# Kernel tuning notes

Measured on AMD Instinct MI355X. Metric: run time of the kernel, lower is better.

Reference implementation:

```python
import jax, jax.numpy as jnp
import numpy as np

SR = 16000
NFFT = 512
HOP = 160
D_MIC = 0.05
SPEED = 343.0
PRE = 0.97
ALPHA, BETA, GAMMA = 0.5, 0.3, 0.2
MAXLEN = 40000
N_ANGLES = 181
T = 6400000

# ---- constant buffers (match torch register_buffer setup) ----
_freqs = np.fft.rfftfreq(NFFT, 1.0 / SR).astype(np.float32)            # [F]
_angles = np.linspace(0.0, 180.0, N_ANGLES).astype(np.float32)         # [A]
_tau = -(D_MIC * np.cos(np.deg2rad(_angles))) / SPEED
_phase = (2.0 * np.pi) * _tau[:, None] * _freqs[None, :]               # [A, F]
STEER_R = jnp.asarray(np.cos(_phase).astype(np.float32))
STEER_I = jnp.asarray(np.sin(_phase).astype(np.float32))
ANGLE_GRID = jnp.asarray(_angles)

_wl = SPEED / (_freqs + 1e-6)
_sr_res = D_MIC / _wl
_spatial = 1.0 / (1.0 + np.exp(-4.0 * (_sr_res - 0.1)))
_fw = 1.0 - np.exp(-((_freqs - SR / 6.0) ** 2) / (2.0 * (SR / 4.0) ** 2))
_alias = np.where(_sr_res < 0.5, np.ones_like(_freqs), np.exp(-2.0 * (_sr_res - 0.5) ** 2))
_cw = (_spatial * _fw * _alias)[None, :]
FREQ_W = jnp.asarray((_cw / (_cw.sum() + 1e-6)).astype(np.float32))    # [1, F]

_w = np.exp(np.linspace(-2.0, 0.0, MAXLEN).astype(np.float32))
TEMPORAL = jnp.asarray((_w / _w.sum()).reshape(1, 1, -1))              # [1,1,MAXLEN]

_n = np.arange(NFFT)
WINDOW = jnp.asarray((0.5 - 0.5 * np.cos(2.0 * np.pi * _n / NFFT)).astype(np.float32))
N_FRAMES = (T - NFFT) // HOP + 1
FRAME_IDX = jnp.asarray((np.arange(N_FRAMES)[:, None] * HOP + _n[None, :]).astype(np.int32))


def _stft(x):
    # x: [1, 1, T] -> (real, imag) each [1, F, n_frames]
    frames = x[:, 0, :][:, FRAME_IDX] * WINDOW       # [1, n_frames, NFFT]
    spec = jnp.fft.rfft(frames, axis=-1)             # [1, n_frames, F]
    spec = jnp.swapaxes(spec, 1, 2)                  # [1, F, n_frames]
    return jnp.real(spec).astype(jnp.float32), jnp.imag(spec).astype(jnp.float32)


def _preproc(w):
    w = w * (1.0 / 32768.0)
    w = w - jnp.mean(w, axis=-1, keepdims=True)
    return jnp.concatenate([w[:, :, :1], w[:, :, 1:] - PRE * w[:, :, :-1]], axis=-1)


def _mvdr_scores(mic_wav_0, mic_wav_1):
    r0, i0 = _stft(_preproc(mic_wav_0))
    r1, i1 = _stft(_preproc(mic_wav_1))
    p0 = r0 * r0 + i0 * i0
    p1 = r1 * r1 + i1 * i1
    r01 = r0 * r1 + i0 * i1
    i01 = i0 * r1 - r0 * i1
    wts = TEMPORAL[..., : p0.shape[-1]]
    R00 = (p0 * wts).sum(2)                          # [1, F]
    R11 = (p1 * wts).sum(2)
    R01r = (r01 * wts).sum(2)
    R01i = (i01 * wts).sum(2)
    trace = (R00 + R11) * 0.5
    det = R00 * R11 - (R01r ** 2 + R01i ** 2) + 1e-6 * trace
    inv_det = 1.0 / det
    iR00 = R11 * inv_det
    iR11 = R00 * inv_det
    iR01r = -R01r * inv_det
    iR01i = -R01i * inv_det
    qf = iR01r * STEER_R + iR01i * STEER_I           # [A, F] (B=1 broadcast)
    qf = iR00 + iR11 + qf + qf
    mvdr = 1.0 / (qf + 1e-6)
    logp = jnp.log(mvdr + 1e-6)
    geometric = jnp.exp((logp * FREQ_W).sum(-1))     # [A]
    arithmetic = (mvdr * FREQ_W).sum(-1)
    peak_w = jax.nn.softmax(mvdr + mvdr, axis=-1)
    peak = (mvdr * peak_w * FREQ_W).sum(-1)
    return ALPHA * geometric + BETA * arithmetic + GAMMA * peak


def setup_inputs() -> dict:
    key = jax.random.key(0)
    k0, k1 = jax.random.split(key)
    mic_wav_0 = jax.random.normal(k0, (1, 1, T), jnp.float32) * 8000.0
    noise = jax.random.normal(k1, (1, 1, T), jnp.float32) * 8000.0
    # correlated second channel with a small time shift (plausible TDOA)
    mic_wav_1 = 0.7 * jnp.roll(mic_wav_0, 3, axis=-1) + 0.3 * noise
    return {"mic_wav_0": mic_wav_0, "mic_wav_1": mic_wav_1}


def reference(mic_wav_0, mic_wav_1):
    scores = _mvdr_scores(mic_wav_0, mic_wav_1)      # [A]
    return ANGLE_GRID[jnp.argmax(scores, axis=-1)]
```

## Files before the change

kernel.cpp:

```cpp
#include <hip/hip_runtime.h>
#include <math.h>

#ifndef M_PI
#define M_PI 3.14159265358979323846
#endif

#define HOP 160
#define NBM 1024
#define NBLK_MAX 1024

__device__ __forceinline__ float wave_reduce(float v) {
    for (int off = 32; off > 0; off >>= 1) v += __shfl_down(v, off, 64);
    return v;
}

__device__ __forceinline__ void dft8(float* xr, float* xi) {
    const float s = 0.70710678118654752440f;
    float t0r = xr[0] + xr[4], t0i = xi[0] + xi[4];
    float t1r = xr[0] - xr[4], t1i = xi[0] - xi[4];
    float t2r = xr[2] + xr[6], t2i = xi[2] + xi[6];
    float t3r = xr[2] - xr[6], t3i = xi[2] - xi[6];
    float E0r = t0r + t2r, E0i = t0i + t2i;
    float E2r = t0r - t2r, E2i = t0i - t2i;
    float E1r = t1r + t3i, E1i = t1i - t3r;
    float E3r = t1r - t3i, E3i = t1i + t3r;
    float u0r = xr[1] + xr[5], u0i = xi[1] + xi[5];
    float u1r = xr[1] - xr[5], u1i = xi[1] - xi[5];
    float u2r = xr[3] + xr[7], u2i = xi[3] + xi[7];
    float u3r = xr[3] - xr[7], u3i = xi[3] - xi[7];
    float O0r = u0r + u2r, O0i = u0i + u2i;
    float O2r = u0r - u2r, O2i = u0i - u2i;
    float O1r = u1r + u3i, O1i = u1i - u3r;
    float O3r = u1r - u3i, O3i = u1i + u3r;
    float T1r = s * (O1r + O1i), T1i = s * (O1i - O1r);
    float T2r = O2i,             T2i = -O2r;
    float T3r = s * (O3i - O3r), T3i = -s * (O3r + O3i);
    xr[0] = E0r + O0r; xi[0] = E0i + O0i;
    xr[4] = E0r - O0r; xi[4] = E0i - O0i;
    xr[1] = E1r + T1r; xi[1] = E1i + T1i;
    xr[5] = E1r - T1r; xi[5] = E1i - T1i;
    xr[2] = E2r + T2r; xi[2] = E2i + T2i;
    xr[6] = E2r - T2r; xi[6] = E2i - T2i;
    xr[3] = E3r + T3r; xi[3] = E3i + T3i;
    xr[7] = E3r - T3r; xi[7] = E3i - T3i;
}

__device__ __forceinline__ void cmul_t(float& zr, float& zi, float tr, float ti) {
    float r = zr * tr - zi * ti;
    float i = zr * ti + zi * tr;
    zr = r; zi = i;
}

__device__ __forceinline__ int stripe(int i) {
    return ((i >> 7) << 8) | (i & 127);
}

__global__ __launch_bounds__(256) void mean_partial_kernel(
        const float* __restrict__ x0, const float* __restrict__ x1,
        float* __restrict__ part, int n, int nbm)
{
    int tid = threadIdx.x;
    float s0 = 0.f, s1 = 0.f;
    int n4 = n >> 2;
    const float4* x04 = (const float4*)x0;
    const float4* x14 = (const float4*)x1;
    for (int i = blockIdx.x * blockDim.x + tid; i < n4; i += blockDim.x * gridDim.x) {
        float4 a = x04[i], b = x14[i];
        s0 += (a.x + a.y) + (a.z + a.w);
        s1 += (b.x + b.y) + (b.z + b.w);
    }
    __shared__ float red[4][2];
    s0 = wave_reduce(s0); s1 = wave_reduce(s1);
    int lane = tid & 63, w = tid >> 6;
    if (lane == 0) { red[w][0] = s0; red[w][1] = s1; }
    __syncthreads();
    if (tid == 0) {
        part[blockIdx.x]       = red[0][0] + red[1][0] + red[2][0] + red[3][0];
        part[nbm + blockIdx.x] = red[0][1] + red[1][1] + red[2][1] + red[3][1];
    }
}

__global__ __launch_bounds__(256) void mean_final_kernel(
        const float* __restrict__ part, float* __restrict__ means,
        float* __restrict__ twd, int n, int nbm)
{
    int tid = threadIdx.x;
    float v0 = 0.f, v1 = 0.f;
    for (int i = tid; i < nbm; i += 256) { v0 += part[i]; v1 += part[nbm + i]; }
    __shared__ float red[4][2];
    v0 = wave_reduce(v0); v1 = wave_reduce(v1);
    int lane = tid & 63, w = tid >> 6;
    if (lane == 0) { red[w][0] = v0; red[w][1] = v1; }
    __syncthreads();
    if (tid == 0) {
        float s0 = red[0][0] + red[1][0] + red[2][0] + red[3][0];
        float s1 = red[0][1] + red[1][1] + red[2][1] + red[3][1];
        float inv = 1.0f / ((float)n * 32768.0f);
        means[0] = s0 * inv;
        means[1] = s1 * inv;
    }
    if (tid < 64) {
        int l = tid, hi = l >> 3;
        for (int j = 0; j < 8; ++j) {
            twd[j * 64 + l] = 0.5f - 0.5f * cosf((float)(2.0 * M_PI / 512.0) * (float)(l + 64 * j));
            float c1, s1v, c2, s2v;
            sincosf((float)(-2.0 * M_PI / 64.0) * (float)(j * hi), &s1v, &c1);
            sincosf((float)(-2.0 * M_PI / 512.0) * (float)(j * l), &s2v, &c2);
            twd[(8 + j) * 64 + l]  = c1;
            twd[(16 + j) * 64 + l] = s1v;
            twd[(24 + j) * 64 + l] = c2;
            twd[(32 + j) * 64 + l] = s2v;
        }
    }
}

__global__ __launch_bounds__(256, 4) void stft_fft_kernel(
        const float* __restrict__ x0, const float* __restrict__ x1,
        const float* __restrict__ means, const float* __restrict__ twd,
        float* __restrict__ partials,
        int nframes, int fpb, int nblocks, float invS, float kslope)
{
    __shared__ float smem[4160];
    const int tid = threadIdx.x;
    const int w = tid >> 6, l = tid & 63;
    float* buf = smem + w * 1024;
    const int n0 = l & 7, hi = l >> 3;
    const int pl = (64 - l) & 63;

    float winv[8], t1r[8], t1i[8], t2r[8], t2i[8];
#pragma unroll
    for (int j = 0; j < 8; ++j) {
        winv[j] = twd[j * 64 + l];
        t1r[j]  = twd[(8 + j) * 64 + l];
        t1i[j]  = twd[(16 + j) * 64 + l];
        t2r[j]  = twd[(24 + j) * 64 + l];
        t2i[j]  = twd[(32 + j) * 64 + l];
    }
    const float m0 = means[0], m1 = means[1];
    const float cm0 = 0.03f * m0, cm1 = 0.03f * m1;
    const float k15 = 1.0f / 32768.0f;

    float A[8];
    float Wr[5], Wi[5];
#pragma unroll
    for (int r = 0; r < 8; ++r) A[r] = 0.f;
#pragma unroll
    for (int r = 0; r < 5; ++r) { Wr[r] = 0.f; Wi[r] = 0.f; }

    int f0 = blockIdx.x * fpb;
    int f1 = f0 + fpb; if (f1 > nframes) f1 = nframes;

    for (int f = f0 + w; f < f1; f += 4) {
        int base = f * HOP;
        float wt = expf(fmaf(kslope, (float)f, -2.0f)) * invS;

        float zr[8], zi[8];
#pragma unroll
        for (int j = 0; j < 8; ++j) {
            int t = base + l + 64 * j;
            int tp = t - 1;
            if (j == 0) tp = (tp < 0) ? 0 : tp;
            float d0 = fmaf(-0.97f, x0[tp], x0[t]);
            float d1 = fmaf(-0.97f, x1[tp], x1[t]);
            float y0 = fmaf(d0, k15, -cm0);
            float y1 = fmaf(d1, k15, -cm1);
            zr[j] = y0 * winv[j];
            zi[j] = y1 * winv[j];
        }

        dft8(zr, zi);

#pragma unroll
        for (int k2 = 0; k2 < 8; ++k2) {
            int a = stripe((l ^ (k2 << 3)) + 64 * k2);
            buf[a] = zr[k2]; buf[a + 128] = zi[k2];
        }
#pragma unroll
        for (int j = 0; j < 8; ++j) {
            int a = stripe(n0 + 8 * (j ^ hi) + 64 * hi);
            zr[j] = buf[a]; zi[j] = buf[a + 128];
        }
#pragma unroll
        for (int j = 1; j < 8; ++j) cmul_t(zr[j], zi[j], t1r[j], t1i[j]);
        dft8(zr, zi);

#pragma unroll
        for (int k1 = 0; k1 < 8; ++k1) {
            int a = stripe(hi + 8 * ((k1 ^ n0) + 8 * n0));
            buf[a] = zr[k1]; buf[a + 128] = zi[k1];
        }
#pragma unroll
        for (int j = 0; j < 8; ++j) {
            int a = stripe(n0 + 8 * ((hi ^ j) + 8 * j));
            zr[j] = buf[a]; zi[j] = buf[a + 128];
        }
#pragma unroll
        for (int j = 1; j < 8; ++j) cmul_t(zr[j], zi[j], t2r[j], t2i[j]);
        dft8(zr, zi);

#pragma unroll
        for (int r = 0; r < 8; ++r) {
            float u = fmaf(zr[r], zr[r], zi[r] * zi[r]);
            A[r] = fmaf(wt, u, A[r]);
        }
#pragma unroll
        for (int r = 0; r < 4; ++r) {
            float br = __shfl(zr[7 - r], pl, 64);
            float bi = __shfl(zi[7 - r], pl, 64);
            if (l == 0) { br = zr[(8 - r) & 7]; bi = zi[(8 - r) & 7]; }
            float wr = fmaf(zr[r], br, -(zi[r] * bi));
            float wi = fmaf(zr[r], bi, zi[r] * br);
            Wr[r] = fmaf(wt, wr, Wr[r]);
            Wi[r] = fmaf(wt, wi, Wi[r]);
        }
        {
            float wr = fmaf(zr[4], zr[4], -(zi[4] * zi[4]));
            float wi = 2.f * zr[4] * zi[4];
            Wr[4] = fmaf(wt, wr, Wr[4]);
            Wi[4] = fmaf(wt, wi, Wi[4]);
        }
    }

    float R00[4], R11[4], R01r[4], R01i[4];
#pragma unroll
    for (int r = 0; r < 4; ++r) {
        float ap = __shfl(A[7 - r], pl, 64);
        if (l == 0) ap = A[(8 - r) & 7];
        R00[r]  = 0.25f * (A[r] + ap + 2.f * Wr[r]);
        R11[r]  = 0.25f * (A[r] + ap - 2.f * Wr[r]);
        R01r[r] = 0.5f  * Wi[r];
        R01i[r] = 0.25f * (A[r] - ap);
    }

    __syncthreads();
    float (*red)[1028] = (float (*)[1028])smem;
#pragma unroll
    for (int r = 0; r < 4; ++r) {
        int k = l + 64 * r;
        red[w][0 * 257 + k] = R00[r];
        red[w][1 * 257 + k] = R11[r];
        red[w][2 * 257 + k] = R01r[r];
        red[w][3 * 257 + k] = R01i[r];
    }
    if (l == 0) {
        red[w][0 * 257 + 256] = 0.5f * (A[4] + Wr[4]);
        red[w][1 * 257 + 256] = 0.5f * (A[4] - Wr[4]);
        red[w][2 * 257 + 256] = 0.5f * Wi[4];
        red[w][3 * 257 + 256] = 0.f;
    }
    __syncthreads();
    for (int s = tid; s < 1028; s += 256) {
        float v = (red[0][s] + red[1][s]) + (red[2][s] + red[3][s]);
        partials[(size_t)s * nblocks + blockIdx.x] = v;
    }
}

__global__ __launch_bounds__(256) void reduce_kernel(
        const float* __restrict__ partials, float* __restrict__ R, int nblocks)
{
    int s = blockIdx.x;
    int tid = threadIdx.x, lane = tid & 63, w = tid >> 6;
    const float* p = partials + (size_t)s * nblocks;
    float v = 0.f;
    for (int i = tid; i < nblocks; i += 256) v += p[i];
    __shared__ float red[4];
    v = wave_reduce(v);
    if (lane == 0) red[w] = v;
    __syncthreads();
    if (tid == 0) R[s] = (red[0] + red[1]) + (red[2] + red[3]);
}

__global__ __launch_bounds__(64) void score_kernel(
        const float* __restrict__ R, float* __restrict__ scores)
{
    int a = blockIdx.x;
    int l = threadIdx.x;

    float rad = (float)a * (float)(M_PI / 180.0);
    float tau = -(0.05f * cosf(rad)) / 343.0f;
    float t2  = (float)(2.0 * M_PI) * tau;

    float fwsum = 0.f;
    float geo = 0.f, ari = 0.f;
    float m = -1e30f, se = 0.f, pe = 0.f;

    for (int q = 0; q < 5; ++q) {
        int kk = l + 64 * q;
        if (kk > 256) break;
        float R00  = R[0 * 257 + kk];
        float R11  = R[1 * 257 + kk];
        float R01r = R[2 * 257 + kk];
        float R01i = R[3 * 257 + kk];
        float trace = (R00 + R11) * 0.5f;
        float det = R00 * R11 - (R01r * R01r + R01i * R01i) + 1e-6f * trace;
        float inv_det = 1.0f / det;
        float Sd = (R11 + R00) * inv_det;
        float qr = -R01r * inv_det;
        float qi = -R01i * inv_det;

        float fq = 31.25f * (float)kk;
        float wl = 343.0f / (fq + 1e-6f);
        float sr = 0.05f / wl;
        float spatial = 1.0f / (1.0f + expf(-4.0f * (sr - 0.1f)));
        float d = fq - (float)(16000.0 / 6.0);
        float fwq = 1.0f - expf(-(d * d) / (float)(2.0 * 4000.0 * 4000.0));
        float alias = (sr < 0.5f) ? 1.0f : expf(-2.0f * (sr - 0.5f) * (sr - 0.5f));
        float fw = spatial * fwq * alias;
        fwsum += fw;

        float cr, ci;
        sincosf(t2 * fq, &ci, &cr);
        float t  = qr * cr + qi * ci;
        float qf = Sd + t + t;
        float mv = 1.0f / (qf + 1e-6f);

        geo = fmaf(logf(mv + 1e-6f), fw, geo);
        ari = fmaf(mv, fw, ari);
        float x = mv + mv;
        if (x > m) {
            float sc = expf(m - x);
            se = fmaf(se, sc, 1.0f);
            pe = fmaf(pe, sc, mv * fw);
            m = x;
        } else {
            float e = expf(x - m);
            se += e;
            pe = fmaf(mv * fw, e, pe);
        }
    }

    for (int off = 1; off < 64; off <<= 1) {
        fwsum += __shfl_xor(fwsum, off, 64);
        geo   += __shfl_xor(geo, off, 64);
        ari   += __shfl_xor(ari, off, 64);
        float mo = __shfl_xor(m, off, 64);
        float so = __shfl_xor(se, off, 64);
        float po = __shfl_xor(pe, off, 64);
        float mm = fmaxf(m, mo);
        float c1 = expf(m - mm), c2 = expf(mo - mm);
        se = fmaf(se, c1, so * c2);
        pe = fmaf(pe, c1, po * c2);
        m = mm;
    }
    if (l == 0) {
        float invcw = 1.0f / (fwsum + 1e-6f);
        float geon = geo * invcw;
        float arin = ari * invcw;
        float peak = (pe * invcw) / se;
        scores[a] = 0.5f * expf(geon) + 0.3f * arin + 0.2f * peak;
    }
}

__global__ __launch_bounds__(256) void argmax_kernel(
        const float* __restrict__ scores, float* __restrict__ out)
{
    int tid = threadIdx.x, lane = tid & 63, w = tid >> 6;
    float v = (tid < 181) ? scores[tid] : -1e30f;
    int   i = tid;
    for (int off = 1; off < 64; off <<= 1) {
        float vo = __shfl_xor(v, off, 64);
        int   io = __shfl_xor(i, off, 64);
        if (vo > v || (vo == v && io < i)) { v = vo; i = io; }
    }
    __shared__ float rv[4];
    __shared__ int   ri[4];
    if (lane == 0) { rv[w] = v; ri[w] = i; }
    __syncthreads();
    if (tid == 0) {
        float bv = rv[0]; int bi = ri[0];
        for (int q = 1; q < 4; ++q) {
            if (rv[q] > bv || (rv[q] == bv && ri[q] < bi)) { bv = rv[q]; bi = ri[q]; }
        }
        out[0] = (float)bi;
    }
}

extern "C" void kernel_launch(void* const* d_in, const int* in_sizes, int n_in,
                              void* d_out, int out_size, void* d_ws, size_t ws_size,
                              hipStream_t stream) {
    const float* x0 = (const float*)d_in[0];
    const float* x1 = (const float*)d_in[1];
    float* out = (float*)d_out;
    int T = in_sizes[0];
    int nframes = (T - 512) / HOP + 1;

    double S = 0.0;
    for (int j = 0; j < 40000; ++j) S += exp(-2.0 + 2.0 * (double)j / 39999.0);
    float invS = (float)(1.0 / S);
    float kslope = (float)(2.0 / 39999.0);

    float* ws = (float*)d_ws;
    float* means    = ws;
    float* twd      = ws + 64;
    float* mpart    = ws + 4096;
    float* Rbuf     = ws + 8192;
    float* scores   = ws + 9472;
    float* partials = ws + 16384;

    long availf = (long)(ws_size / 4) - 16384;
    int nblocks = (int)(availf / 1028);
    if (nblocks > NBLK_MAX) nblocks = NBLK_MAX;
    if (nblocks < 1) nblocks = 1;
    int fpb = (nframes + nblocks - 1) / nblocks;

    mean_partial_kernel<<<NBM, 256, 0, stream>>>(x0, x1, mpart, T, NBM);
    mean_final_kernel<<<1, 256, 0, stream>>>(mpart, means, twd, T, NBM);
    stft_fft_kernel<<<nblocks, 256, 0, stream>>>(x0, x1, means, twd, partials,
                                                 nframes, fpb, nblocks, invS, kslope);
    reduce_kernel<<<1028, 256, 0, stream>>>(partials, Rbuf, nblocks);
    score_kernel<<<181, 64, 0, stream>>>(Rbuf, scores);
    argmax_kernel<<<1, 256, 0, stream>>>(scores, out);
}
```

Before: 84.79 us.

## Fuse mean pass into STFT kernel and apply DC correction analytically in scoring

Removes the separate mean-reduction and twiddle-setup kernels. Each STFT block now sums its own chunk of the raw signal, and the STFT runs on the un-centred signal. The mean's effect on the covariance (only the DC bins and the window's neighbouring bins) is corrected afterwards in score_kernel, using accumulated weighted linear spectra and the total weight. Twiddles are now built by in-register recurrence from one sincos instead of table loads, and blocks and occupancy go up (NBLK_MAX 2048, launch bounds 256,8). This cuts one full pass over the input and two launches, at the cost of extra correction algebra and possible float accuracy drift from the twiddle recurrence and the uncentred FFT.

```diff
diff --git a/kernel.cpp b/kernel.cpp
--- a/kernel.cpp
+++ b/kernel.cpp
@@ -6,8 +6,8 @@
 #endif
 
 #define HOP 160
-#define NBM 1024
-#define NBLK_MAX 1024
+#define NBLK_MAX 2048
+#define PSLOTS 1036
 
 __device__ __forceinline__ float wave_reduce(float v) {
     for (int off = 32; off > 0; off >>= 1) v += __shfl_down(v, off, 64);
@@ -55,93 +55,44 @@
     return ((i >> 7) << 8) | (i & 127);
 }
 
-__global__ __launch_bounds__(256) void mean_partial_kernel(
+__global__ __launch_bounds__(256, 8) void stft_fft_kernel(
         const float* __restrict__ x0, const float* __restrict__ x1,
-        float* __restrict__ part, int n, int nbm)
+        float* __restrict__ partials,
+        int T, int nframes, int fpb, int nblocks, int cs,
+        float invS, float kslope)
 {
-    int tid = threadIdx.x;
-    float s0 = 0.f, s1 = 0.f;
-    int n4 = n >> 2;
-    const float4* x04 = (const float4*)x0;
-    const float4* x14 = (const float4*)x1;
-    for (int i = blockIdx.x * blockDim.x + tid; i < n4; i += blockDim.x * gridDim.x) {
-        float4 a = x04[i], b = x14[i];
-        s0 += (a.x + a.y) + (a.z + a.w);
-        s1 += (b.x + b.y) + (b.z + b.w);
-    }
-    __shared__ float red[4][2];
-    s0 = wave_reduce(s0); s1 = wave_reduce(s1);
-    int lane = tid & 63, w = tid >> 6;
-    if (lane == 0) { red[w][0] = s0; red[w][1] = s1; }
-    __syncthreads();
-    if (tid == 0) {
-        part[blockIdx.x]       = red[0][0] + red[1][0] + red[2][0] + red[3][0];
-        part[nbm + blockIdx.x] = red[0][1] + red[1][1] + red[2][1] + red[3][1];
-    }
-}
-
-__global__ __launch_bounds__(256) void mean_final_kernel(
-        const float* __restrict__ part, float* __restrict__ means,
-        float* __restrict__ twd, int n, int nbm)
-{
-    int tid = threadIdx.x;
-    float v0 = 0.f, v1 = 0.f;
-    for (int i = tid; i < nbm; i += 256) { v0 += part[i]; v1 += part[nbm + i]; }
-    __shared__ float red[4][2];
-    v0 = wave_reduce(v0); v1 = wave_reduce(v1);
-    int lane = tid & 63, w = tid >> 6;
-    if (lane == 0) { red[w][0] = v0; red[w][1] = v1; }
-    __syncthreads();
-    if (tid == 0) {
-        float s0 = red[0][0] + red[1][0] + red[2][0] + red[3][0];
-        float s1 = red[0][1] + red[1][1] + red[2][1] + red[3][1];
-        float inv = 1.0f / ((float)n * 32768.0f);
-        means[0] = s0 * inv;
-        means[1] = s1 * inv;
-    }
-    if (tid < 64) {
-        int l = tid, hi = l >> 3;
-        for (int j = 0; j < 8; ++j) {
-            twd[j * 64 + l] = 0.5f - 0.5f * cosf((float)(2.0 * M_PI / 512.0) * (float)(l + 64 * j));
-            float c1, s1v, c2, s2v;
-            sincosf((float)(-2.0 * M_PI / 64.0) * (float)(j * hi), &s1v, &c1);
-            sincosf((float)(-2.0 * M_PI / 512.0) * (float)(j * l), &s2v, &c2);
-            twd[(8 + j) * 64 + l]  = c1;
-            twd[(16 + j) * 64 + l] = s1v;
-            twd[(24 + j) * 64 + l] = c2;
-            twd[(32 + j) * 64 + l] = s2v;
-        }
-    }
-}
-
-__global__ __launch_bounds__(256, 4) void stft_fft_kernel(
-        const float* __restrict__ x0, const float* __restrict__ x1,
-        const float* __restrict__ means, const float* __restrict__ twd,
-        float* __restrict__ partials,
-        int nframes, int fpb, int nblocks, float invS, float kslope)
-{
-    __shared__ float smem[4160];
+    __shared__ float smem[4 * PSLOTS];
     const int tid = threadIdx.x;
     const int w = tid >> 6, l = tid & 63;
     float* buf = smem + w * 1024;
     const int n0 = l & 7, hi = l >> 3;
     const int pl = (64 - l) & 63;
 
-    float winv[8], t1r[8], t1i[8], t2r[8], t2i[8];
-#pragma unroll
-    for (int j = 0; j < 8; ++j) {
-        winv[j] = twd[j * 64 + l];
-        t1r[j]  = twd[(8 + j) * 64 + l];
-        t1i[j]  = twd[(16 + j) * 64 + l];
-        t2r[j]  = twd[(24 + j) * 64 + l];
-        t2i[j]  = twd[(32 + j) * 64 + l];
-    }
-    const float m0 = means[0], m1 = means[1];
-    const float cm0 = 0.03f * m0, cm1 = 0.03f * m1;
-    const float k15 = 1.0f / 32768.0f;
+    float c0 = 0.f, c1 = 0.f;
+    {
+        int lo = blockIdx.x * cs;
+        int hi2 = lo + cs; if (hi2 > T) hi2 = T;
+        for (int i = lo + tid; i < hi2; i += 256) { c0 += x0[i]; c1 += x1[i]; }
+        c0 = wave_reduce(c0); c1 = wave_reduce(c1);
+        if (l == 0) { smem[2 * w] = c0; smem[2 * w + 1] = c1; }
+    }
+    __syncthreads();
+    const float c0T = (smem[0] + smem[2]) + (smem[4] + smem[6]);
+    const float c1T = (smem[1] + smem[3]) + (smem[5] + smem[7]);
+    __syncthreads();
+
+    float winv[8];
+#pragma unroll
+    for (int j = 0; j < 8; ++j)
+        winv[j] = (0.5f - 0.5f * cosf((float)(2.0 * M_PI / 512.0) * (float)(l + 64 * j)))
+                  * (1.0f / 32768.0f);
+    float g1r, g1i, g2r, g2i;
+    sincosf((float)(-2.0 * M_PI / 64.0) * (float)hi, &g1i, &g1r);
+    sincosf((float)(-2.0 * M_PI / 512.0) * (float)l, &g2i, &g2r);
 
     float A[8];
     float Wr[5], Wi[5];
+    float L0r = 0.f, L0i = 0.f, L7r = 0.f, L7i = 0.f;
 #pragma unroll
     for (int r = 0; r < 8; ++r) A[r] = 0.f;
 #pragma unroll
@@ -162,10 +113,8 @@
             if (j == 0) tp = (tp < 0) ? 0 : tp;
             float d0 = fmaf(-0.97f, x0[tp], x0[t]);
             float d1 = fmaf(-0.97f, x1[tp], x1[t]);
-            float y0 = fmaf(d0, k15, -cm0);
-            float y1 = fmaf(d1, k15, -cm1);
-            zr[j] = y0 * winv[j];
-            zi[j] = y1 * winv[j];
+            zr[j] = d0 * winv[j];
+            zi[j] = d1 * winv[j];
         }
 
         dft8(zr, zi);
@@ -180,8 +129,18 @@
             int a = stripe(n0 + 8 * (j ^ hi) + 64 * hi);
             zr[j] = buf[a]; zi[j] = buf[a + 128];
         }
-#pragma unroll
-        for (int j = 1; j < 8; ++j) cmul_t(zr[j], zi[j], t1r[j], t1i[j]);
+        {
+            float rc = g1r, rs = g1i;
+#pragma unroll
+            for (int j = 1; j < 8; ++j) {
+                cmul_t(zr[j], zi[j], rc, rs);
+                if (j < 7) {
+                    float nr = rc * g1r - rs * g1i;
+                    rs = fmaf(rc, g1i, rs * g1r);
+                    rc = nr;
+                }
+            }
+        }
         dft8(zr, zi);
 
 #pragma unroll
@@ -194,8 +153,18 @@
             int a = stripe(n0 + 8 * ((hi ^ j) + 8 * j));
             zr[j] = buf[a]; zi[j] = buf[a + 128];
         }
-#pragma unroll
-        for (int j = 1; j < 8; ++j) cmul_t(zr[j], zi[j], t2r[j], t2i[j]);
+        {
+            float rc = g2r, rs = g2i;
+#pragma unroll
+            for (int j = 1; j < 8; ++j) {
+                cmul_t(zr[j], zi[j], rc, rs);
+                if (j < 7) {
+                    float nr = rc * g2r - rs * g2i;
+                    rs = fmaf(rc, g2i, rs * g2r);
+                    rc = nr;
+                }
+            }
+        }
         dft8(zr, zi);
 
 #pragma unroll
@@ -203,6 +172,9 @@
             float u = fmaf(zr[r], zr[r], zi[r] * zi[r]);
             A[r] = fmaf(wt, u, A[r]);
         }
+        L0r = fmaf(wt, zr[0], L0r); L0i = fmaf(wt, zi[0], L0i);
+        L7r = fmaf(wt, zr[7], L7r); L7i = fmaf(wt, zi[7], L7i);
+
 #pragma unroll
         for (int r = 0; r < 4; ++r) {
             float br = __shfl(zr[7 - r], pl, 64);
@@ -233,7 +205,7 @@
     }
 
     __syncthreads();
-    float (*red)[1028] = (float (*)[1028])smem;
+    float (*red)[PSLOTS] = (float (*)[PSLOTS])smem;
 #pragma unroll
     for (int r = 0; r < 4; ++r) {
         int k = l + 64 * r;
@@ -247,10 +219,23 @@
         red[w][1 * 257 + 256] = 0.5f * (A[4] - Wr[4]);
         red[w][2 * 257 + 256] = 0.5f * Wi[4];
         red[w][3 * 257 + 256] = 0.f;
-    }
-    __syncthreads();
-    for (int s = tid; s < 1028; s += 256) {
+        red[w][1028] = L0r;
+        red[w][1029] = L0i;
+    }
+    if (l == 1) {
+        red[w][1030] = L0r;
+        red[w][1031] = L0i;
+    }
+    if (l == 63) {
+        red[w][1032] = L7r;
+        red[w][1033] = L7i;
+    }
+    if (l == 2) { red[w][1034] = 0.f; red[w][1035] = 0.f; }
+    __syncthreads();
+    for (int s = tid; s < PSLOTS; s += 256) {
         float v = (red[0][s] + red[1][s]) + (red[2][s] + red[3][s]);
+        if (s == 1034) v = c0T;
+        if (s == 1035) v = c1T;
         partials[(size_t)s * nblocks + blockIdx.x] = v;
     }
 }
@@ -271,7 +256,8 @@
 }
 
 __global__ __launch_bounds__(64) void score_kernel(
-        const float* __restrict__ R, float* __restrict__ scores)
+        const float* __restrict__ R, float* __restrict__ scores,
+        float Sw, float invT32768)
 {
     int a = blockIdx.x;
     int l = threadIdx.x;
@@ -279,6 +265,12 @@
     float rad = (float)a * (float)(M_PI / 180.0);
     float tau = -(0.05f * cosf(rad)) / 343.0f;
     float t2  = (float)(2.0 * M_PI) * tau;
+
+    float dr = 0.03f * R[1034] * invT32768;
+    float di = 0.03f * R[1035] * invT32768;
+    float dd  = dr * dr + di * di;
+    float d2r = dr * dr - di * di;
+    float d2i = 2.f * dr * di;
 
     float fwsum = 0.f;
     float geo = 0.f, ari = 0.f;
@@ -291,6 +283,32 @@
         float R11  = R[1 * 257 + kk];
         float R01r = R[2 * 257 + kk];
         float R01i = R[3 * 257 + kk];
+
+        if (q == 0 && l == 0) {
+            float Lr = R[1028], Li = R[1029];
+            float dA  = -512.f * (dr * Lr + di * Li) + 65536.f * dd * Sw;
+            float dLr = dr * Lr - di * Li;
+            float dLi = dr * Li + di * Lr;
+            float dWr = -512.f * dLr + 65536.f * Sw * d2r;
+            float dWi = -512.f * dLi + 65536.f * Sw * d2i;
+            R00  += 0.5f * (dA + dWr);
+            R11  += 0.5f * (dA - dWr);
+            R01r += 0.5f * dWi;
+        }
+        if (q == 0 && l == 1) {
+            float L1r = R[1030], L1i = R[1031];
+            float L5r = R[1032], L5i = R[1033];
+            float dA1 = 256.f * (dr * L1r + di * L1i) + 16384.f * dd * Sw;
+            float dA5 = 256.f * (dr * L5r + di * L5i) + 16384.f * dd * Sw;
+            float Sr = L1r + L5r, Si = L1i + L5i;
+            float dWr = 128.f * (dr * Sr - di * Si) + 16384.f * Sw * d2r;
+            float dWi = 128.f * (dr * Si + di * Sr) + 16384.f * Sw * d2i;
+            R00  += 0.25f * (dA1 + dA5 + 2.f * dWr);
+            R11  += 0.25f * (dA1 + dA5 - 2.f * dWr);
+            R01r += 0.5f  * dWi;
+            R01i += 0.25f * (dA1 - dA5);
+        }
+
         float trace = (R00 + R11) * 0.5f;
         float det = R00 * R11 - (R01r * R01r + R01i * R01i) + 1e-6f * trace;
         float inv_det = 1.0f / det;
@@ -302,8 +320,8 @@
         float wl = 343.0f / (fq + 1e-6f);
         float sr = 0.05f / wl;
         float spatial = 1.0f / (1.0f + expf(-4.0f * (sr - 0.1f)));
-        float d = fq - (float)(16000.0 / 6.0);
-        float fwq = 1.0f - expf(-(d * d) / (float)(2.0 * 4000.0 * 4000.0));
+        float dq = fq - (float)(16000.0 / 6.0);
+        float fwq = 1.0f - expf(-(dq * dq) / (float)(2.0 * 4000.0 * 4000.0));
         float alias = (sr < 0.5f) ? 1.0f : expf(-2.0f * (sr - 0.5f) * (sr - 0.5f));
         float fw = spatial * fwq * alias;
         fwsum += fw;
@@ -337,9 +355,9 @@
         float so = __shfl_xor(se, off, 64);
         float po = __shfl_xor(pe, off, 64);
         float mm = fmaxf(m, mo);
-        float c1 = expf(m - mm), c2 = expf(mo - mm);
-        se = fmaf(se, c1, so * c2);
-        pe = fmaf(pe, c1, po * c2);
+        float e1 = expf(m - mm), e2 = expf(mo - mm);
+        se = fmaf(se, e1, so * e2);
+        pe = fmaf(pe, e1, po * e2);
         m = mm;
     }
     if (l == 0) {
@@ -384,30 +402,33 @@
     int T = in_sizes[0];
     int nframes = (T - 512) / HOP + 1;
 
-    double S = 0.0;
-    for (int j = 0; j < 40000; ++j) S += exp(-2.0 + 2.0 * (double)j / 39999.0);
-    float invS = (float)(1.0 / S);
+    double Stot = 0.0, Spart = 0.0;
+    for (int j = 0; j < 40000; ++j) {
+        double e = exp(-2.0 + 2.0 * (double)j / 39999.0);
+        Stot += e;
+        if (j < nframes) Spart += e;
+    }
+    float invS = (float)(1.0 / Stot);
     float kslope = (float)(2.0 / 39999.0);
+    float Sw = (float)(Spart / Stot);
+    float invT32768 = (float)(1.0 / ((double)T * 32768.0));
 
     float* ws = (float*)d_ws;
-    float* means    = ws;
-    float* twd      = ws + 64;
-    float* mpart    = ws + 4096;
-    float* Rbuf     = ws + 8192;
-    float* scores   = ws + 9472;
-    float* partials = ws + 16384;
-
-    long availf = (long)(ws_size / 4) - 16384;
-    int nblocks = (int)(availf / 1028);
+    float* Rbuf     = ws;
+    float* scores   = ws + 2048;
+    float* partials = ws + 4096;
+
+    long availf = (long)(ws_size / 4) - 4096;
+    int nblocks = (int)(availf / PSLOTS);
     if (nblocks > NBLK_MAX) nblocks = NBLK_MAX;
     if (nblocks < 1) nblocks = 1;
     int fpb = (nframes + nblocks - 1) / nblocks;
-
-    mean_partial_kernel<<<NBM, 256, 0, stream>>>(x0, x1, mpart, T, NBM);
-    mean_final_kernel<<<1, 256, 0, stream>>>(mpart, means, twd, T, NBM);
-    stft_fft_kernel<<<nblocks, 256, 0, stream>>>(x0, x1, means, twd, partials,
-                                                 nframes, fpb, nblocks, invS, kslope);
-    reduce_kernel<<<1028, 256, 0, stream>>>(partials, Rbuf, nblocks);
-    score_kernel<<<181, 64, 0, stream>>>(Rbuf, scores);
+    int cs  = (T + nblocks - 1) / nblocks;
+
+    stft_fft_kernel<<<nblocks, 256, 0, stream>>>(x0, x1, partials,
+                                                 T, nframes, fpb, nblocks, cs,
+                                                 invS, kslope);
+    reduce_kernel<<<PSLOTS, 256, 0, stream>>>(partials, Rbuf, nblocks);
+    score_kernel<<<181, 64, 0, stream>>>(Rbuf, scores, Sw, invT32768);
     argmax_kernel<<<1, 256, 0, stream>>>(scores, out);
 }
```

Measured after the change: 193.1 us. +127.7%, slower.
